# Optimization experiments

Hardware: AMD Instinct MI355X
Metric: run time of the kernel (lower is better)

Reference implementation:

```python
import jax, jax.numpy as jnp
import numpy as np
import math

N = 100000      # active voxels
K = 27          # 3**3 kernel offsets
L = 50000
INC = 64
OUTC = 64


def setup_inputs() -> dict:
    key = jax.random.key(0)
    k1, k2, k3, k4 = jax.random.split(key, 4)
    features = jax.random.normal(k1, (N, INC), dtype=jnp.float32)
    # kernel init: uniform(-std, std), std = 1/sqrt(inc * k^3)
    std = 1.0 / math.sqrt(INC * K)
    kernel = jax.random.uniform(k2, (K, INC, OUTC), dtype=jnp.float32,
                                minval=-std, maxval=std)
    neighbor_in = jax.random.randint(k3, (K, L), 0, N, dtype=jnp.int32)
    neighbor_out = jax.random.randint(k4, (K, L), 0, N, dtype=jnp.int32)
    return {"features": features, "kernel": kernel,
            "neighbor_in": neighbor_in, "neighbor_out": neighbor_out}


def reference(features, kernel, neighbor_in, neighbor_out):
    # gather -> per-offset GEMM -> scatter-add (torchsparse sparseconv_op, transpose=False)
    gathered = features[neighbor_in]                      # [K, L, INC]
    vals = jnp.einsum('klc,kco->klo', gathered, kernel)    # [K, L, OUTC]
    out = jnp.zeros((features.shape[0], kernel.shape[-1]), dtype=features.dtype)
    out = out.at[neighbor_out.reshape(-1)].add(vals.reshape(-1, kernel.shape[-1]))
    return out
```

## Files before the change

kernel.cpp:

```cpp
#include <hip/hip_runtime.h>
#include <hip/hip_bf16.h>


typedef __bf16 bf16x8 __attribute__((ext_vector_type(8)));
typedef float f32x4 __attribute__((ext_vector_type(4)));

#define KOFF 27
#define SLOTK 4
#define NSLOT (KOFF * SLOTK)
#define OVFCAP 8192
#define WPAD 72
#define ROWCHUNK 8192
#define NIBW (ROWCHUNK / 8)

__global__ __launch_bounds__(256) void kA_rank_cast(
    const float* __restrict__ feat, const float* __restrict__ kern,
    const int* __restrict__ nout, __bf16* __restrict__ fb,
    __bf16* __restrict__ wt, unsigned short* __restrict__ slots,
    int2* __restrict__ ovf, int* __restrict__ ovfcnt, int Lpairs, int nElems,
    int nchunk, int rankBlocks, int wtBlocks) {
  __shared__ unsigned int nib[NIBW];
  if ((int)blockIdx.x < rankBlocks) {
    const int k = blockIdx.x / nchunk;
    const int chunk = blockIdx.x % nchunk;
    const int lo = chunk * ROWCHUNK;
    const int tid = threadIdx.x;
    for (int i = tid; i < NIBW; i += 256) nib[i] = 0u;
    __syncthreads();
    const int* nk = nout + k * Lpairs;
    for (int base = 0; base < Lpairs; base += 2048) {
      int l[8], row[8];
#pragma unroll
      for (int j = 0; j < 8; ++j) {
        l[j] = base + j * 256 + tid;
        row[j] = (l[j] < Lpairs) ? nk[l[j]] : -1;
      }
#pragma unroll
      for (int j = 0; j < 8; ++j) {
        int rr = row[j] - lo;
        if (rr >= 0 && rr < ROWCHUNK) {
          unsigned int sh = ((unsigned)rr & 7u) * 4u;
          unsigned int old = atomicAdd(&nib[rr >> 3], 1u << sh);
          int rank = (old >> sh) & 15;
          if (rank < SLOTK) {
            slots[(size_t)row[j] * NSLOT + k * SLOTK + rank] =
                (unsigned short)l[j];
          } else {
            int idx = atomicAdd(ovfcnt, 1);
            if (idx < OVFCAP) ovf[idx] = make_int2(row[j], k * Lpairs + l[j]);
          }
        }
      }
    }
  } else if ((int)blockIdx.x < rankBlocks + wtBlocks) {
    int kc = (blockIdx.x - rankBlocks) * 256 + threadIdx.x;
    if (kc < KOFF * 64) {
      int k = kc >> 6, c = kc & 63;
      const float* src = kern + k * 4096 + c;
      __bf16* dst = wt + (size_t)kc * 64;
#pragma unroll
      for (int i0 = 0; i0 < 64; i0 += 8) {
        bf16x8 v;
#pragma unroll
        for (int q = 0; q < 8; ++q) v[q] = (__bf16)src[(i0 + q) * 64];
        *(bf16x8*)(dst + i0) = v;
      }
    }
  } else {
    int i = ((blockIdx.x - rankBlocks - wtBlocks) * 256 + threadIdx.x) * 8;
    if (i < nElems) {
      f32x4 a = *(const f32x4*)(feat + i);
      f32x4 b = *(const f32x4*)(feat + i + 4);
      bf16x8 v;
#pragma unroll
      for (int j = 0; j < 4; ++j) {
        v[j] = (__bf16)a[j];
        v[j + 4] = (__bf16)b[j];
      }
      *(bf16x8*)(fb + i) = v;
    }
  }
}

__global__ __launch_bounds__(256) void kF_fused(
    const __bf16* __restrict__ fb, const __bf16* __restrict__ wt,
    const int* __restrict__ nin, const unsigned short* __restrict__ slots,
    float* __restrict__ out, int Lpairs, int Nrows) {
  __shared__ __bf16 ldsW[2][64 * WPAD];
  const int tid = threadIdx.x;
  const int wv = tid >> 6, lane = tid & 63;
  const int r = lane & 15, g = lane >> 4;
  int row = blockIdx.x * 64 + wv * 16 + r;
  if (row >= Nrows) row = Nrows - 1;
  const unsigned short* srow = slots + (size_t)row * NSLOT;

  const int sc = tid >> 2;
  const int si = (tid & 3) * 16;

  {
    const __bf16* wp = wt + sc * 64 + si;
    bf16x8 wa = *(const bf16x8*)(wp);
    bf16x8 wb = *(const bf16x8*)(wp + 8);
    *(bf16x8*)&ldsW[0][sc * WPAD + si] = wa;
    *(bf16x8*)&ldsW[0][sc * WPAD + si + 8] = wb;
  }

  uint2 sv0 = *(const uint2*)(srow);
  uint2 sv1 = *(const uint2*)(srow + SLOTK);
  int e[4] = {(int)(sv0.x & 0xFFFF), (int)(sv0.x >> 16),
              (int)(sv0.y & 0xFFFF), (int)(sv0.y >> 16)};
  int en[4] = {(int)(sv1.x & 0xFFFF), (int)(sv1.x >> 16),
               (int)(sv1.y & 0xFFFF), (int)(sv1.y >> 16)};
  int irow[4], irown[4];
#pragma unroll
  for (int j = 0; j < 4; ++j) irow[j] = (e[j] != 0xFFFF) ? nin[e[j]] : -1;

  f32x4 acc[4] = {f32x4{0.f, 0.f, 0.f, 0.f}, f32x4{0.f, 0.f, 0.f, 0.f},
                  f32x4{0.f, 0.f, 0.f, 0.f}, f32x4{0.f, 0.f, 0.f, 0.f}};
  __syncthreads();

  for (int k = 0; k < KOFF; ++k) {
    const int kb = k & 1;
    bf16x8 fa[4], fc[4];
#pragma unroll
    for (int j = 0; j < 4; ++j) {
      if (irow[j] >= 0) {
        const __bf16* ap = fb + (size_t)irow[j] * 64 + g * 8;
        fa[j] = *(const bf16x8*)(ap);
        fc[j] = *(const bf16x8*)(ap + 32);
      }
    }
    const int* ninK1 = nin + (k + 1) * Lpairs;
#pragma unroll
    for (int j = 0; j < 4; ++j)
      irown[j] = (k + 1 < KOFF && en[j] != 0xFFFF) ? ninK1[en[j]] : -1;
    uint2 sv2 = make_uint2(0xFFFFFFFFu, 0xFFFFFFFFu);
    if (k + 2 < KOFF) sv2 = *(const uint2*)(srow + (k + 2) * SLOTK);
    if (k + 1 < KOFF) {
      const __bf16* wp = wt + (size_t)(k + 1) * 4096 + sc * 64 + si;
      bf16x8 wa = *(const bf16x8*)(wp);
      bf16x8 wb = *(const bf16x8*)(wp + 8);
      *(bf16x8*)&ldsW[kb ^ 1][sc * WPAD + si] = wa;
      *(bf16x8*)&ldsW[kb ^ 1][sc * WPAD + si + 8] = wb;
    }
    float s0[8] = {0.f, 0.f, 0.f, 0.f, 0.f, 0.f, 0.f, 0.f};
    float s1[8] = {0.f, 0.f, 0.f, 0.f, 0.f, 0.f, 0.f, 0.f};
#pragma unroll
    for (int j = 0; j < 4; ++j) {
      if (irow[j] >= 0) {
#pragma unroll
        for (int q = 0; q < 8; ++q) {
          s0[q] += (float)fa[j][q];
          s1[q] += (float)fc[j][q];
        }
      }
    }
    bf16x8 b0, b1;
#pragma unroll
    for (int q = 0; q < 8; ++q) {
      b0[q] = (__bf16)s0[q];
      b1[q] = (__bf16)s1[q];
    }
    bf16x8 w0f[4], w1f[4];
#pragma unroll
    for (int t = 0; t < 4; ++t) {
      w0f[t] = *(const bf16x8*)&ldsW[kb][(t * 16 + r) * WPAD + g * 8];
      w1f[t] = *(const bf16x8*)&ldsW[kb][(t * 16 + r) * WPAD + g * 8 + 32];
    }
#pragma unroll
    for (int t = 0; t < 4; ++t) {
      acc[t] = __builtin_amdgcn_mfma_f32_16x16x32_bf16(w0f[t], b0, acc[t], 0, 0, 0);
      acc[t] = __builtin_amdgcn_mfma_f32_16x16x32_bf16(w1f[t], b1, acc[t], 0, 0, 0);
    }
    __syncthreads();
#pragma unroll
    for (int j = 0; j < 4; ++j) irow[j] = irown[j];
    en[0] = (int)(sv2.x & 0xFFFF);
    en[1] = (int)(sv2.x >> 16);
    en[2] = (int)(sv2.y & 0xFFFF);
    en[3] = (int)(sv2.y >> 16);
  }

  float* op = out + (size_t)row * 64;
#pragma unroll
  for (int t = 0; t < 4; ++t) *(f32x4*)(op + t * 16 + g * 4) = acc[t];
}

__global__ __launch_bounds__(256) void k4_fixup(
    const __bf16* __restrict__ fb, const __bf16* __restrict__ wt,
    const int* __restrict__ nin, const int2* __restrict__ ovf,
    const int* __restrict__ ovfcnt, float* __restrict__ out, int Lpairs) {
  int gid = blockIdx.x * 256 + threadIdx.x;
  int i = gid >> 6, c = gid & 63;
  int n = *ovfcnt;
  if (n > OVFCAP) n = OVFCAP;
  if (i >= n) return;
  int row = ovf[i].x, pid = ovf[i].y;
  int k = pid / Lpairs;
  int irow = nin[pid];
  const __bf16* wk = wt + ((size_t)k * 64 + c) * 64;
  const __bf16* f = fb + (size_t)irow * 64;
  float s = 0.f;
#pragma unroll 8
  for (int q = 0; q < 64; ++q) s += (float)f[q] * (float)wk[q];
  atomicAdd(&out[(size_t)row * 64 + c], s);
}

__global__ __launch_bounds__(256) void spconv_atomic_kernel(
    const float* __restrict__ feat, const float* __restrict__ kern,
    const int* __restrict__ nin, const int* __restrict__ nout,
    float* __restrict__ out, int Lpairs, int blocksPerK) {
  __shared__ __bf16 ldsBT[64 * WPAD];
  const int bk = blockIdx.x / blocksPerK;
  const int chunk = blockIdx.x % blocksPerK;
  const float* kb = kern + bk * 4096;
  for (int idx = threadIdx.x; idx < 4096; idx += 256) {
    int i = idx >> 6, c = idx & 63;
    ldsBT[c * WPAD + i] = (__bf16)kb[idx];
  }
  __syncthreads();
  const int lane = threadIdx.x & 63;
  const int wave = threadIdx.x >> 6;
  const int r = lane & 15, g = lane >> 4;
  bf16x8 bfrag[2][4];
#pragma unroll
  for (int s = 0; s < 2; ++s)
#pragma unroll
    for (int t = 0; t < 4; ++t)
      bfrag[s][t] = *(const bf16x8*)&ldsBT[(t * 16 + r) * WPAD + g * 8 + s * 32];
  const int* ninK = nin + bk * Lpairs;
  const int* noutK = nout + bk * Lpairs;
  const int base0 = chunk * 512 + wave * 128;
  for (int it = 0; it < 8; ++it) {
    const int base = base0 + it * 16;
    if (base >= Lpairs) break;
    const int arow = ninK[base + r];
    const float* ap = feat + (size_t)arow * 64 + g * 8;
    f32x4 f0 = *(const f32x4*)(ap);
    f32x4 f1 = *(const f32x4*)(ap + 4);
    f32x4 f2 = *(const f32x4*)(ap + 32);
    f32x4 f3 = *(const f32x4*)(ap + 36);
    bf16x8 a0, a1;
#pragma unroll
    for (int j = 0; j < 4; ++j) {
      a0[j] = (__bf16)f0[j];
      a0[j + 4] = (__bf16)f1[j];
      a1[j] = (__bf16)f2[j];
      a1[j + 4] = (__bf16)f3[j];
    }
    f32x4 acc[4] = {f32x4{0.f, 0.f, 0.f, 0.f}, f32x4{0.f, 0.f, 0.f, 0.f},
                    f32x4{0.f, 0.f, 0.f, 0.f}, f32x4{0.f, 0.f, 0.f, 0.f}};
#pragma unroll
    for (int t = 0; t < 4; ++t) {
      acc[t] = __builtin_amdgcn_mfma_f32_16x16x32_bf16(a0, bfrag[0][t], acc[t], 0, 0, 0);
      acc[t] = __builtin_amdgcn_mfma_f32_16x16x32_bf16(a1, bfrag[1][t], acc[t], 0, 0, 0);
    }
    int orow[4];
#pragma unroll
    for (int reg = 0; reg < 4; ++reg) orow[reg] = noutK[base + g * 4 + reg];
#pragma unroll
    for (int t = 0; t < 4; ++t)
#pragma unroll
      for (int reg = 0; reg < 4; ++reg)
        atomicAdd(out + (size_t)orow[reg] * 64 + t * 16 + r, acc[t][reg]);
  }
}

extern "C" void kernel_launch(void* const* d_in, const int* in_sizes, int n_in,
                              void* d_out, int out_size, void* d_ws, size_t ws_size,
                              hipStream_t stream) {
  const float* feat = (const float*)d_in[0];
  const float* kern = (const float*)d_in[1];
  const int* nin = (const int*)d_in[2];
  const int* nout = (const int*)d_in[3];
  float* out = (float*)d_out;

  const int total = in_sizes[2];
  const int Lpairs = total / KOFF;
  const int Nrows = out_size / 64;
  const int nElems = Nrows * 64;

  const size_t slotsBytes = (size_t)Nrows * NSLOT * 2;
  const size_t ovfOff = (slotsBytes + 255) & ~(size_t)255;
  const size_t cntOff = (ovfOff + (size_t)OVFCAP * 8 + 255) & ~(size_t)255;
  const size_t wtOff = (cntOff + 256 + 255) & ~(size_t)255;
  const size_t fbOff = (wtOff + (size_t)KOFF * 4096 * 2 + 255) & ~(size_t)255;
  const size_t needed = fbOff + (size_t)nElems * 2;

  const bool shapeOK = (Lpairs <= 65535) && (Lpairs % 16 == 0) &&
                       (total % KOFF == 0) && (out_size % 64 == 0);

  if (shapeOK && ws_size >= needed) {
    unsigned short* slots = (unsigned short*)d_ws;
    int2* ovf = (int2*)((char*)d_ws + ovfOff);
    int* ovfcnt = (int*)((char*)d_ws + cntOff);
    __bf16* wt = (__bf16*)((char*)d_ws + wtOff);
    __bf16* fb = (__bf16*)((char*)d_ws + fbOff);

    hipMemsetAsync(slots, 0xFF, slotsBytes, stream);
    hipMemsetAsync(ovfcnt, 0, 4, stream);

    const int nchunk = (Nrows + ROWCHUNK - 1) / ROWCHUNK;
    const int rankBlocks = KOFF * nchunk;
    const int wtBlocks = (KOFF * 64 + 255) / 256;
    const int castBlocks = (nElems / 8 + 255) / 256;
    kA_rank_cast<<<rankBlocks + wtBlocks + castBlocks, 256, 0, stream>>>(
        feat, kern, nout, fb, wt, slots, ovf, ovfcnt, Lpairs, nElems, nchunk,
        rankBlocks, wtBlocks);
    kF_fused<<<(Nrows + 63) / 64, 256, 0, stream>>>(fb, wt, nin, slots, out,
                                                    Lpairs, Nrows);
    k4_fixup<<<OVFCAP * 64 / 256, 256, 0, stream>>>(fb, wt, nin, ovf, ovfcnt,
                                                    out, Lpairs);
  } else {
    const int blocksPerK = (Lpairs + 511) / 512;
    hipMemsetAsync(d_out, 0, (size_t)out_size * sizeof(float), stream);
    spconv_atomic_kernel<<<KOFF * blocksPerK, 256, 0, stream>>>(
        feat, kern, nin, nout, out, Lpairs, blocksPerK);
  }
}
```

Measured before the change: 135.4 us.

## Pre-swizzle weights into MFMA fragment layout and load from global, dropping LDS staging

The weight-prep stage now writes the bf16 kernel directly in per-lane MFMA fragment order, so each lane of the fused kernel loads its weight fragments with contiguous 16-byte global loads. The LDS double buffer and the per-offset __syncthreads are removed, and weights are register-double-buffered across an unrolled-by-two offset loop. This aims to cut LDS traffic and block-wide barriers in the main loop. In exchange every wave re-reads the weights from global memory or cache and register pressure rises. The overflow fixup now reads fp32 weights straight from the original kernel tensor.

```diff
diff --git a/kernel.cpp b/kernel.cpp
--- a/kernel.cpp
+++ b/kernel.cpp
@@ -16,7 +16,7 @@
 __global__ __launch_bounds__(256) void kA_rank_cast(
     const float* __restrict__ feat, const float* __restrict__ kern,
     const int* __restrict__ nout, __bf16* __restrict__ fb,
-    __bf16* __restrict__ wt, unsigned short* __restrict__ slots,
+    __bf16* __restrict__ wtf, unsigned short* __restrict__ slots,
     int2* __restrict__ ovf, int* __restrict__ ovfcnt, int Lpairs, int nElems,
     int nchunk, int rankBlocks, int wtBlocks) {
   __shared__ unsigned int nib[NIBW];
@@ -53,18 +53,19 @@
       }
     }
   } else if ((int)blockIdx.x < rankBlocks + wtBlocks) {
-    int kc = (blockIdx.x - rankBlocks) * 256 + threadIdx.x;
-    if (kc < KOFF * 64) {
-      int k = kc >> 6, c = kc & 63;
-      const float* src = kern + k * 4096 + c;
-      __bf16* dst = wt + (size_t)kc * 64;
-#pragma unroll
-      for (int i0 = 0; i0 < 64; i0 += 8) {
-        bf16x8 v;
-#pragma unroll
-        for (int q = 0; q < 8; ++q) v[q] = (__bf16)src[(i0 + q) * 64];
-        *(bf16x8*)(dst + i0) = v;
-      }
+    int idx = (blockIdx.x - rankBlocks) * 256 + threadIdx.x;
+    if (idx < KOFF * 512) {
+      int k = idx >> 9;
+      int rem = idx & 511;
+      int s = rem >> 8;
+      int t = (rem >> 6) & 3;
+      int lane = rem & 63;
+      int g = lane >> 4, r = lane & 15;
+      const float* src = kern + k * 4096 + (s * 32 + g * 8) * 64 + (t * 16 + r);
+      bf16x8 v;
+#pragma unroll
+      for (int q = 0; q < 8; ++q) v[q] = (__bf16)src[q * 64];
+      *(bf16x8*)(wtf + (size_t)idx * 8) = v;
     }
   } else {
     int i = ((blockIdx.x - rankBlocks - wtBlocks) * 256 + threadIdx.x) * 8;
@@ -83,27 +84,16 @@
 }
 
 __global__ __launch_bounds__(256) void kF_fused(
-    const __bf16* __restrict__ fb, const __bf16* __restrict__ wt,
+    const __bf16* __restrict__ fb, const __bf16* __restrict__ wtf,
     const int* __restrict__ nin, const unsigned short* __restrict__ slots,
     float* __restrict__ out, int Lpairs, int Nrows) {
-  __shared__ __bf16 ldsW[2][64 * WPAD];
   const int tid = threadIdx.x;
   const int wv = tid >> 6, lane = tid & 63;
   const int r = lane & 15, g = lane >> 4;
   int row = blockIdx.x * 64 + wv * 16 + r;
   if (row >= Nrows) row = Nrows - 1;
   const unsigned short* srow = slots + (size_t)row * NSLOT;
-
-  const int sc = tid >> 2;
-  const int si = (tid & 3) * 16;
-
-  {
-    const __bf16* wp = wt + sc * 64 + si;
-    bf16x8 wa = *(const bf16x8*)(wp);
-    bf16x8 wb = *(const bf16x8*)(wp + 8);
-    *(bf16x8*)&ldsW[0][sc * WPAD + si] = wa;
-    *(bf16x8*)&ldsW[0][sc * WPAD + si + 8] = wb;
-  }
+  const __bf16* wl = wtf + lane * 8;
 
   uint2 sv0 = *(const uint2*)(srow);
   uint2 sv1 = *(const uint2*)(srow + SLOTK);
@@ -117,10 +107,16 @@
 
   f32x4 acc[4] = {f32x4{0.f, 0.f, 0.f, 0.f}, f32x4{0.f, 0.f, 0.f, 0.f},
                   f32x4{0.f, 0.f, 0.f, 0.f}, f32x4{0.f, 0.f, 0.f, 0.f}};
-  __syncthreads();
-
-  for (int k = 0; k < KOFF; ++k) {
-    const int kb = k & 1;
+
+  auto loadW = [&](int k, bf16x8(&w0)[4], bf16x8(&w1)[4]) {
+    const __bf16* wp = wl + (size_t)k * 4096;
+#pragma unroll
+    for (int t = 0; t < 4; ++t) w0[t] = *(const bf16x8*)(wp + t * 512);
+#pragma unroll
+    for (int t = 0; t < 4; ++t) w1[t] = *(const bf16x8*)(wp + 2048 + t * 512);
+  };
+
+  auto body = [&](int k, bf16x8(&w0)[4], bf16x8(&w1)[4]) {
     bf16x8 fa[4], fc[4];
 #pragma unroll
     for (int j = 0; j < 4; ++j) {
@@ -136,13 +132,7 @@
       irown[j] = (k + 1 < KOFF && en[j] != 0xFFFF) ? ninK1[en[j]] : -1;
     uint2 sv2 = make_uint2(0xFFFFFFFFu, 0xFFFFFFFFu);
     if (k + 2 < KOFF) sv2 = *(const uint2*)(srow + (k + 2) * SLOTK);
-    if (k + 1 < KOFF) {
-      const __bf16* wp = wt + (size_t)(k + 1) * 4096 + sc * 64 + si;
-      bf16x8 wa = *(const bf16x8*)(wp);
-      bf16x8 wb = *(const bf16x8*)(wp + 8);
-      *(bf16x8*)&ldsW[kb ^ 1][sc * WPAD + si] = wa;
-      *(bf16x8*)&ldsW[kb ^ 1][sc * WPAD + si + 8] = wb;
-    }
+
     float s0[8] = {0.f, 0.f, 0.f, 0.f, 0.f, 0.f, 0.f, 0.f};
     float s1[8] = {0.f, 0.f, 0.f, 0.f, 0.f, 0.f, 0.f, 0.f};
 #pragma unroll
@@ -161,25 +151,28 @@
       b0[q] = (__bf16)s0[q];
       b1[q] = (__bf16)s1[q];
     }
-    bf16x8 w0f[4], w1f[4];
 #pragma unroll
     for (int t = 0; t < 4; ++t) {
-      w0f[t] = *(const bf16x8*)&ldsW[kb][(t * 16 + r) * WPAD + g * 8];
-      w1f[t] = *(const bf16x8*)&ldsW[kb][(t * 16 + r) * WPAD + g * 8 + 32];
-    }
-#pragma unroll
-    for (int t = 0; t < 4; ++t) {
-      acc[t] = __builtin_amdgcn_mfma_f32_16x16x32_bf16(w0f[t], b0, acc[t], 0, 0, 0);
-      acc[t] = __builtin_amdgcn_mfma_f32_16x16x32_bf16(w1f[t], b1, acc[t], 0, 0, 0);
-    }
-    __syncthreads();
+      acc[t] = __builtin_amdgcn_mfma_f32_16x16x32_bf16(w0[t], b0, acc[t], 0, 0, 0);
+      acc[t] = __builtin_amdgcn_mfma_f32_16x16x32_bf16(w1[t], b1, acc[t], 0, 0, 0);
+    }
 #pragma unroll
     for (int j = 0; j < 4; ++j) irow[j] = irown[j];
     en[0] = (int)(sv2.x & 0xFFFF);
     en[1] = (int)(sv2.x >> 16);
     en[2] = (int)(sv2.y & 0xFFFF);
     en[3] = (int)(sv2.y >> 16);
-  }
+  };
+
+  bf16x8 wA0[4], wA1[4], wB0[4], wB1[4];
+  loadW(0, wA0, wA1);
+  for (int k = 0; k < KOFF - 1; k += 2) {
+    loadW(k + 1, wB0, wB1);
+    body(k, wA0, wA1);
+    loadW(k + 2, wA0, wA1);
+    body(k + 1, wB0, wB1);
+  }
+  body(KOFF - 1, wA0, wA1);
 
   float* op = out + (size_t)row * 64;
 #pragma unroll
@@ -187,7 +180,7 @@
 }
 
 __global__ __launch_bounds__(256) void k4_fixup(
-    const __bf16* __restrict__ fb, const __bf16* __restrict__ wt,
+    const __bf16* __restrict__ fb, const float* __restrict__ kern,
     const int* __restrict__ nin, const int2* __restrict__ ovf,
     const int* __restrict__ ovfcnt, float* __restrict__ out, int Lpairs) {
   int gid = blockIdx.x * 256 + threadIdx.x;
@@ -197,12 +190,12 @@
   if (i >= n) return;
   int row = ovf[i].x, pid = ovf[i].y;
   int k = pid / Lpairs;
-  int irow = nin[pid];
-  const __bf16* wk = wt + ((size_t)k * 64 + c) * 64;
-  const __bf16* f = fb + (size_t)irow * 64;
+  int irowv = nin[pid];
+  const float* wk = kern + k * 4096 + c;
+  const __bf16* f = fb + (size_t)irowv * 64;
   float s = 0.f;
 #pragma unroll 8
-  for (int q = 0; q < 64; ++q) s += (float)f[q] * (float)wk[q];
+  for (int q = 0; q < 64; ++q) s += (float)f[q] * wk[q * 64];
   atomicAdd(&out[(size_t)row * 64 + c], s);
 }
 
@@ -294,7 +287,7 @@
     unsigned short* slots = (unsigned short*)d_ws;
     int2* ovf = (int2*)((char*)d_ws + ovfOff);
     int* ovfcnt = (int*)((char*)d_ws + cntOff);
-    __bf16* wt = (__bf16*)((char*)d_ws + wtOff);
+    __bf16* wtf = (__bf16*)((char*)d_ws + wtOff);
     __bf16* fb = (__bf16*)((char*)d_ws + fbOff);
 
     hipMemsetAsync(slots, 0xFF, slotsBytes, stream);
@@ -302,14 +295,14 @@
 
     const int nchunk = (Nrows + ROWCHUNK - 1) / ROWCHUNK;
     const int rankBlocks = KOFF * nchunk;
-    const int wtBlocks = (KOFF * 64 + 255) / 256;
+    const int wtBlocks = (KOFF * 512 + 255) / 256;
     const int castBlocks = (nElems / 8 + 255) / 256;
     kA_rank_cast<<<rankBlocks + wtBlocks + castBlocks, 256, 0, stream>>>(
-        feat, kern, nout, fb, wt, slots, ovf, ovfcnt, Lpairs, nElems, nchunk,
+        feat, kern, nout, fb, wtf, slots, ovf, ovfcnt, Lpairs, nElems, nchunk,
         rankBlocks, wtBlocks);
-    kF_fused<<<(Nrows + 63) / 64, 256, 0, stream>>>(fb, wt, nin, slots, out,
+    kF_fused<<<(Nrows + 63) / 64, 256, 0, stream>>>(fb, wtf, nin, slots, out,
                                                     Lpairs, Nrows);
-    k4_fixup<<<OVFCAP * 64 / 256, 256, 0, stream>>>(fb, wt, nin, ovf, ovfcnt,
+    k4_fixup<<<OVFCAP * 64 / 256, 256, 0, stream>>>(fb, kern, nin, ovf, ovfcnt,
                                                     out, Lpairs);
   } else {
     const int blocksPerK = (Lpairs + 511) / 512;
```

Measured after the change: 162.5 us. 1.2x slower.

## Deepen gather pipeline by prefetching next offset's features one iteration ahead

Applied to the files above, without the earlier changes.

Restructures the per-offset loop so that the feature rows for offset k+1 are loaded while offset k is being reduced and multiplied, with neighbor indices resolved two offsets ahead. Register buffers are ping-ponged through a lambda called twice per loop iteration. The weight tile is staged in registers and written to LDS after the MFMAs, with the barrier moved there. The aim is to hide gather latency behind compute, at the cost of more live registers and a possible occupancy drop.

```diff
diff --git a/kernel.cpp b/kernel.cpp
--- a/kernel.cpp
+++ b/kernel.cpp
@@ -107,51 +107,69 @@
 
   uint2 sv0 = *(const uint2*)(srow);
   uint2 sv1 = *(const uint2*)(srow + SLOTK);
-  int e[4] = {(int)(sv0.x & 0xFFFF), (int)(sv0.x >> 16),
-              (int)(sv0.y & 0xFFFF), (int)(sv0.y >> 16)};
-  int en[4] = {(int)(sv1.x & 0xFFFF), (int)(sv1.x >> 16),
+  uint2 sv2 = *(const uint2*)(srow + 2 * SLOTK);
+  int e0[4] = {(int)(sv0.x & 0xFFFF), (int)(sv0.x >> 16),
+               (int)(sv0.y & 0xFFFF), (int)(sv0.y >> 16)};
+  int e1[4] = {(int)(sv1.x & 0xFFFF), (int)(sv1.x >> 16),
                (int)(sv1.y & 0xFFFF), (int)(sv1.y >> 16)};
-  int irow[4], irown[4];
-#pragma unroll
-  for (int j = 0; j < 4; ++j) irow[j] = (e[j] != 0xFFFF) ? nin[e[j]] : -1;
+  int enN[4] = {(int)(sv2.x & 0xFFFF), (int)(sv2.x >> 16),
+                (int)(sv2.y & 0xFFFF), (int)(sv2.y >> 16)};
+  int gA[4], gB[4], irowNxt[4];
+#pragma unroll
+  for (int j = 0; j < 4; ++j) gA[j] = (e0[j] != 0xFFFF) ? nin[e0[j]] : -1;
+  const int* nin1 = nin + Lpairs;
+#pragma unroll
+  for (int j = 0; j < 4; ++j) irowNxt[j] = (e1[j] != 0xFFFF) ? nin1[e1[j]] : -1;
 
   f32x4 acc[4] = {f32x4{0.f, 0.f, 0.f, 0.f}, f32x4{0.f, 0.f, 0.f, 0.f},
                   f32x4{0.f, 0.f, 0.f, 0.f}, f32x4{0.f, 0.f, 0.f, 0.f}};
+
   __syncthreads();
 
-  for (int k = 0; k < KOFF; ++k) {
+  bf16x8 faA[4], fcA[4], faB[4], fcB[4];
+#pragma unroll
+  for (int j = 0; j < 4; ++j) {
+    if (gA[j] >= 0) {
+      const __bf16* ap = fb + (size_t)gA[j] * 64 + g * 8;
+      faA[j] = *(const bf16x8*)(ap);
+      fcA[j] = *(const bf16x8*)(ap + 32);
+    }
+  }
+
+  auto body = [&](int k, bf16x8(&faC)[4], bf16x8(&fcC)[4], int(&gC)[4],
+                  bf16x8(&faN)[4], bf16x8(&fcN)[4], int(&gN)[4]) {
     const int kb = k & 1;
-    bf16x8 fa[4], fc[4];
-#pragma unroll
-    for (int j = 0; j < 4; ++j) {
-      if (irow[j] >= 0) {
-        const __bf16* ap = fb + (size_t)irow[j] * 64 + g * 8;
-        fa[j] = *(const bf16x8*)(ap);
-        fc[j] = *(const bf16x8*)(ap + 32);
-      }
-    }
-    const int* ninK1 = nin + (k + 1) * Lpairs;
-#pragma unroll
-    for (int j = 0; j < 4; ++j)
-      irown[j] = (k + 1 < KOFF && en[j] != 0xFFFF) ? ninK1[en[j]] : -1;
-    uint2 sv2 = make_uint2(0xFFFFFFFFu, 0xFFFFFFFFu);
-    if (k + 2 < KOFF) sv2 = *(const uint2*)(srow + (k + 2) * SLOTK);
+    bf16x8 wa, wb;
     if (k + 1 < KOFF) {
       const __bf16* wp = wt + (size_t)(k + 1) * 4096 + sc * 64 + si;
-      bf16x8 wa = *(const bf16x8*)(wp);
-      bf16x8 wb = *(const bf16x8*)(wp + 8);
-      *(bf16x8*)&ldsW[kb ^ 1][sc * WPAD + si] = wa;
-      *(bf16x8*)&ldsW[kb ^ 1][sc * WPAD + si + 8] = wb;
-    }
+      wa = *(const bf16x8*)(wp);
+      wb = *(const bf16x8*)(wp + 8);
+    }
+#pragma unroll
+    for (int j = 0; j < 4; ++j) gN[j] = irowNxt[j];
+#pragma unroll
+    for (int j = 0; j < 4; ++j) {
+      if (gN[j] >= 0) {
+        const __bf16* ap = fb + (size_t)gN[j] * 64 + g * 8;
+        faN[j] = *(const bf16x8*)(ap);
+        fcN[j] = *(const bf16x8*)(ap + 32);
+      }
+    }
+    const int* nin2 = nin + (size_t)(k + 2) * Lpairs;
+#pragma unroll
+    for (int j = 0; j < 4; ++j)
+      irowNxt[j] = (k + 2 < KOFF && enN[j] != 0xFFFF) ? nin2[enN[j]] : -1;
+    uint2 sv3 = make_uint2(0xFFFFFFFFu, 0xFFFFFFFFu);
+    if (k + 3 < KOFF) sv3 = *(const uint2*)(srow + (k + 3) * SLOTK);
     float s0[8] = {0.f, 0.f, 0.f, 0.f, 0.f, 0.f, 0.f, 0.f};
     float s1[8] = {0.f, 0.f, 0.f, 0.f, 0.f, 0.f, 0.f, 0.f};
 #pragma unroll
     for (int j = 0; j < 4; ++j) {
-      if (irow[j] >= 0) {
+      if (gC[j] >= 0) {
 #pragma unroll
         for (int q = 0; q < 8; ++q) {
-          s0[q] += (float)fa[j][q];
-          s1[q] += (float)fc[j][q];
+          s0[q] += (float)faC[j][q];
+          s1[q] += (float)fcC[j][q];
         }
       }
     }
@@ -172,14 +190,22 @@
       acc[t] = __builtin_amdgcn_mfma_f32_16x16x32_bf16(w0f[t], b0, acc[t], 0, 0, 0);
       acc[t] = __builtin_amdgcn_mfma_f32_16x16x32_bf16(w1f[t], b1, acc[t], 0, 0, 0);
     }
-    __syncthreads();
-#pragma unroll
-    for (int j = 0; j < 4; ++j) irow[j] = irown[j];
-    en[0] = (int)(sv2.x & 0xFFFF);
-    en[1] = (int)(sv2.x >> 16);
-    en[2] = (int)(sv2.y & 0xFFFF);
-    en[3] = (int)(sv2.y >> 16);
-  }
+    if (k + 1 < KOFF) {
+      *(bf16x8*)&ldsW[kb ^ 1][sc * WPAD + si] = wa;
+      *(bf16x8*)&ldsW[kb ^ 1][sc * WPAD + si + 8] = wb;
+      __syncthreads();
+    }
+    enN[0] = (int)(sv3.x & 0xFFFF);
+    enN[1] = (int)(sv3.x >> 16);
+    enN[2] = (int)(sv3.y & 0xFFFF);
+    enN[3] = (int)(sv3.y >> 16);
+  };
+
+  for (int k = 0; k + 1 < KOFF; k += 2) {
+    body(k, faA, fcA, gA, faB, fcB, gB);
+    body(k + 1, faB, fcB, gB, faA, fcA, gA);
+  }
+  body(KOFF - 1, faA, fcA, gA, faB, fcB, gB);
 
   float* op = out + (size_t)row * 64;
 #pragma unroll
```

After: 138.6 us. 2.4% more time.

## Process two 16-row tiles per wave in fused sparse conv kernel

Applied to the files above, without the earlier changes.

Each wave now handles 32 output rows as two 16-row MFMA tiles, so every block covers 128 rows and the grid is halved. Each weight fragment loaded from LDS feeds twice as many MFMAs, and the per-offset weight staging and barrier cost is spread over more rows. The next offset's weights are now held in registers and written to LDS after the MFMAs, with the barrier skipped on the last offset. This doubles the gather loads in flight per thread and raises register pressure, and with half as many blocks (about 780) there may be fewer waves to hide gather latency.

```diff
diff --git a/kernel.cpp b/kernel.cpp
--- a/kernel.cpp
+++ b/kernel.cpp
@@ -90,9 +90,12 @@
   const int tid = threadIdx.x;
   const int wv = tid >> 6, lane = tid & 63;
   const int r = lane & 15, g = lane >> 4;
-  int row = blockIdx.x * 64 + wv * 16 + r;
-  if (row >= Nrows) row = Nrows - 1;
-  const unsigned short* srow = slots + (size_t)row * NSLOT;
+  int row0 = blockIdx.x * 128 + wv * 32 + r;
+  int row1 = row0 + 16;
+  if (row0 >= Nrows) row0 = Nrows - 1;
+  if (row1 >= Nrows) row1 = Nrows - 1;
+  const unsigned short* srow0 = slots + (size_t)row0 * NSLOT;
+  const unsigned short* srow1 = slots + (size_t)row1 * NSLOT;
 
   const int sc = tid >> 2;
   const int si = (tid & 3) * 16;
@@ -105,61 +108,99 @@
     *(bf16x8*)&ldsW[0][sc * WPAD + si + 8] = wb;
   }
 
-  uint2 sv0 = *(const uint2*)(srow);
-  uint2 sv1 = *(const uint2*)(srow + SLOTK);
-  int e[4] = {(int)(sv0.x & 0xFFFF), (int)(sv0.x >> 16),
-              (int)(sv0.y & 0xFFFF), (int)(sv0.y >> 16)};
-  int en[4] = {(int)(sv1.x & 0xFFFF), (int)(sv1.x >> 16),
-               (int)(sv1.y & 0xFFFF), (int)(sv1.y >> 16)};
-  int irow[4], irown[4];
-#pragma unroll
-  for (int j = 0; j < 4; ++j) irow[j] = (e[j] != 0xFFFF) ? nin[e[j]] : -1;
-
-  f32x4 acc[4] = {f32x4{0.f, 0.f, 0.f, 0.f}, f32x4{0.f, 0.f, 0.f, 0.f},
-                  f32x4{0.f, 0.f, 0.f, 0.f}, f32x4{0.f, 0.f, 0.f, 0.f}};
+  uint2 s0a = *(const uint2*)(srow0);
+  uint2 s0b = *(const uint2*)(srow0 + SLOTK);
+  uint2 s1a = *(const uint2*)(srow1);
+  uint2 s1b = *(const uint2*)(srow1 + SLOTK);
+  int en0[4] = {(int)(s0b.x & 0xFFFF), (int)(s0b.x >> 16),
+                (int)(s0b.y & 0xFFFF), (int)(s0b.y >> 16)};
+  int en1[4] = {(int)(s1b.x & 0xFFFF), (int)(s1b.x >> 16),
+                (int)(s1b.y & 0xFFFF), (int)(s1b.y >> 16)};
+  int e0[4] = {(int)(s0a.x & 0xFFFF), (int)(s0a.x >> 16),
+               (int)(s0a.y & 0xFFFF), (int)(s0a.y >> 16)};
+  int e1[4] = {(int)(s1a.x & 0xFFFF), (int)(s1a.x >> 16),
+               (int)(s1a.y & 0xFFFF), (int)(s1a.y >> 16)};
+  int irow0[4], irow1[4], irown0[4], irown1[4];
+#pragma unroll
+  for (int j = 0; j < 4; ++j) {
+    irow0[j] = (e0[j] != 0xFFFF) ? nin[e0[j]] : -1;
+    irow1[j] = (e1[j] != 0xFFFF) ? nin[e1[j]] : -1;
+  }
+
+  f32x4 acc0[4] = {f32x4{0.f, 0.f, 0.f, 0.f}, f32x4{0.f, 0.f, 0.f, 0.f},
+                   f32x4{0.f, 0.f, 0.f, 0.f}, f32x4{0.f, 0.f, 0.f, 0.f}};
+  f32x4 acc1[4] = {f32x4{0.f, 0.f, 0.f, 0.f}, f32x4{0.f, 0.f, 0.f, 0.f},
+                   f32x4{0.f, 0.f, 0.f, 0.f}, f32x4{0.f, 0.f, 0.f, 0.f}};
   __syncthreads();
 
   for (int k = 0; k < KOFF; ++k) {
     const int kb = k & 1;
-    bf16x8 fa[4], fc[4];
-#pragma unroll
-    for (int j = 0; j < 4; ++j) {
-      if (irow[j] >= 0) {
-        const __bf16* ap = fb + (size_t)irow[j] * 64 + g * 8;
-        fa[j] = *(const bf16x8*)(ap);
-        fc[j] = *(const bf16x8*)(ap + 32);
-      }
-    }
-    const int* ninK1 = nin + (k + 1) * Lpairs;
-#pragma unroll
-    for (int j = 0; j < 4; ++j)
-      irown[j] = (k + 1 < KOFF && en[j] != 0xFFFF) ? ninK1[en[j]] : -1;
-    uint2 sv2 = make_uint2(0xFFFFFFFFu, 0xFFFFFFFFu);
-    if (k + 2 < KOFF) sv2 = *(const uint2*)(srow + (k + 2) * SLOTK);
+    bf16x8 wa, wb;
     if (k + 1 < KOFF) {
       const __bf16* wp = wt + (size_t)(k + 1) * 4096 + sc * 64 + si;
-      bf16x8 wa = *(const bf16x8*)(wp);
-      bf16x8 wb = *(const bf16x8*)(wp + 8);
-      *(bf16x8*)&ldsW[kb ^ 1][sc * WPAD + si] = wa;
-      *(bf16x8*)&ldsW[kb ^ 1][sc * WPAD + si + 8] = wb;
-    }
-    float s0[8] = {0.f, 0.f, 0.f, 0.f, 0.f, 0.f, 0.f, 0.f};
-    float s1[8] = {0.f, 0.f, 0.f, 0.f, 0.f, 0.f, 0.f, 0.f};
-#pragma unroll
-    for (int j = 0; j < 4; ++j) {
-      if (irow[j] >= 0) {
+      wa = *(const bf16x8*)(wp);
+      wb = *(const bf16x8*)(wp + 8);
+    }
+    bf16x8 fa0[4], fc0[4], fa1[4], fc1[4];
+#pragma unroll
+    for (int j = 0; j < 4; ++j) {
+      if (irow0[j] >= 0) {
+        const __bf16* ap = fb + (size_t)irow0[j] * 64 + g * 8;
+        fa0[j] = *(const bf16x8*)(ap);
+        fc0[j] = *(const bf16x8*)(ap + 32);
+      }
+    }
+#pragma unroll
+    for (int j = 0; j < 4; ++j) {
+      if (irow1[j] >= 0) {
+        const __bf16* ap = fb + (size_t)irow1[j] * 64 + g * 8;
+        fa1[j] = *(const bf16x8*)(ap);
+        fc1[j] = *(const bf16x8*)(ap + 32);
+      }
+    }
+    const int* nin1 = nin + (size_t)(k + 1) * Lpairs;
+#pragma unroll
+    for (int j = 0; j < 4; ++j) {
+      irown0[j] = (k + 1 < KOFF && en0[j] != 0xFFFF) ? nin1[en0[j]] : -1;
+      irown1[j] = (k + 1 < KOFF && en1[j] != 0xFFFF) ? nin1[en1[j]] : -1;
+    }
+    uint2 sv20 = make_uint2(0xFFFFFFFFu, 0xFFFFFFFFu);
+    uint2 sv21 = make_uint2(0xFFFFFFFFu, 0xFFFFFFFFu);
+    if (k + 2 < KOFF) {
+      sv20 = *(const uint2*)(srow0 + (k + 2) * SLOTK);
+      sv21 = *(const uint2*)(srow1 + (k + 2) * SLOTK);
+    }
+    float p00[8] = {0.f, 0.f, 0.f, 0.f, 0.f, 0.f, 0.f, 0.f};
+    float p01[8] = {0.f, 0.f, 0.f, 0.f, 0.f, 0.f, 0.f, 0.f};
+#pragma unroll
+    for (int j = 0; j < 4; ++j) {
+      if (irow0[j] >= 0) {
 #pragma unroll
         for (int q = 0; q < 8; ++q) {
-          s0[q] += (float)fa[j][q];
-          s1[q] += (float)fc[j][q];
+          p00[q] += (float)fa0[j][q];
+          p01[q] += (float)fc0[j][q];
         }
       }
     }
-    bf16x8 b0, b1;
+    float p10[8] = {0.f, 0.f, 0.f, 0.f, 0.f, 0.f, 0.f, 0.f};
+    float p11[8] = {0.f, 0.f, 0.f, 0.f, 0.f, 0.f, 0.f, 0.f};
+#pragma unroll
+    for (int j = 0; j < 4; ++j) {
+      if (irow1[j] >= 0) {
+#pragma unroll
+        for (int q = 0; q < 8; ++q) {
+          p10[q] += (float)fa1[j][q];
+          p11[q] += (float)fc1[j][q];
+        }
+      }
+    }
+    bf16x8 b00, b01, b10, b11;
 #pragma unroll
     for (int q = 0; q < 8; ++q) {
-      b0[q] = (__bf16)s0[q];
-      b1[q] = (__bf16)s1[q];
+      b00[q] = (__bf16)p00[q];
+      b01[q] = (__bf16)p01[q];
+      b10[q] = (__bf16)p10[q];
+      b11[q] = (__bf16)p11[q];
     }
     bf16x8 w0f[4], w1f[4];
 #pragma unroll
@@ -169,21 +210,37 @@
     }
 #pragma unroll
     for (int t = 0; t < 4; ++t) {
-      acc[t] = __builtin_amdgcn_mfma_f32_16x16x32_bf16(w0f[t], b0, acc[t], 0, 0, 0);
-      acc[t] = __builtin_amdgcn_mfma_f32_16x16x32_bf16(w1f[t], b1, acc[t], 0, 0, 0);
-    }
-    __syncthreads();
-#pragma unroll
-    for (int j = 0; j < 4; ++j) irow[j] = irown[j];
-    en[0] = (int)(sv2.x & 0xFFFF);
-    en[1] = (int)(sv2.x >> 16);
-    en[2] = (int)(sv2.y & 0xFFFF);
-    en[3] = (int)(sv2.y >> 16);
-  }
-
-  float* op = out + (size_t)row * 64;
-#pragma unroll
-  for (int t = 0; t < 4; ++t) *(f32x4*)(op + t * 16 + g * 4) = acc[t];
+      acc0[t] = __builtin_amdgcn_mfma_f32_16x16x32_bf16(w0f[t], b00, acc0[t], 0, 0, 0);
+      acc0[t] = __builtin_amdgcn_mfma_f32_16x16x32_bf16(w1f[t], b01, acc0[t], 0, 0, 0);
+      acc1[t] = __builtin_amdgcn_mfma_f32_16x16x32_bf16(w0f[t], b10, acc1[t], 0, 0, 0);
+      acc1[t] = __builtin_amdgcn_mfma_f32_16x16x32_bf16(w1f[t], b11, acc1[t], 0, 0, 0);
+    }
+    if (k + 1 < KOFF) {
+      *(bf16x8*)&ldsW[kb ^ 1][sc * WPAD + si] = wa;
+      *(bf16x8*)&ldsW[kb ^ 1][sc * WPAD + si + 8] = wb;
+      __syncthreads();
+    }
+#pragma unroll
+    for (int j = 0; j < 4; ++j) {
+      irow0[j] = irown0[j];
+      irow1[j] = irown1[j];
+    }
+    en0[0] = (int)(sv20.x & 0xFFFF);
+    en0[1] = (int)(sv20.x >> 16);
+    en0[2] = (int)(sv20.y & 0xFFFF);
+    en0[3] = (int)(sv20.y >> 16);
+    en1[0] = (int)(sv21.x & 0xFFFF);
+    en1[1] = (int)(sv21.x >> 16);
+    en1[2] = (int)(sv21.y & 0xFFFF);
+    en1[3] = (int)(sv21.y >> 16);
+  }
+
+  float* op0 = out + (size_t)row0 * 64;
+  float* op1 = out + (size_t)row1 * 64;
+#pragma unroll
+  for (int t = 0; t < 4; ++t) *(f32x4*)(op0 + t * 16 + g * 4) = acc0[t];
+#pragma unroll
+  for (int t = 0; t < 4; ++t) *(f32x4*)(op1 + t * 16 + g * 4) = acc1[t];
 }
 
 __global__ __launch_bounds__(256) void k4_fixup(
@@ -307,8 +364,8 @@
     kA_rank_cast<<<rankBlocks + wtBlocks + castBlocks, 256, 0, stream>>>(
         feat, kern, nout, fb, wt, slots, ovf, ovfcnt, Lpairs, nElems, nchunk,
         rankBlocks, wtBlocks);
-    kF_fused<<<(Nrows + 63) / 64, 256, 0, stream>>>(fb, wt, nin, slots, out,
-                                                    Lpairs, Nrows);
+    kF_fused<<<(Nrows + 127) / 128, 256, 0, stream>>>(fb, wt, nin, slots, out,
+                                                      Lpairs, Nrows);
     k4_fixup<<<OVFCAP * 64 / 256, 256, 0, stream>>>(fb, wt, nin, ovf, ovfcnt,
                                                     out, Lpairs);
   } else {
```

New measurement: 149.9 us. +10.7%, slower.
